# Kernel optimization log

Measured on AMD Instinct MI355X. Metric: run time of the kernel, lower is better.

Reference implementation:

```python
import jax, jax.numpy as jnp
import numpy as np

T, B, C, K, E = 1024, 32, 1024, 1024, 16  # seq, batch, d_model(=in=out), key_dim, n_experts
LOSS_SCALE = 0.01


def setup_inputs() -> dict:
    key0 = jax.random.key(0)
    k0, k1, k2, k3 = jax.random.split(key0, 4)
    x = jax.random.normal(k0, (T, B, C), dtype=jnp.float32)
    key = jax.random.normal(k1, (1, B, K), dtype=jnp.float32)
    bnd = float(np.sqrt(6.0 / (K + E)))  # xavier_uniform for assign Linear
    assign_w = jax.random.uniform(k2, (K, E), jnp.float32, -bnd, bnd)
    assign_b = jnp.zeros((E,), jnp.float32)
    a = float(np.sqrt(6.0) / (C + C))  # dynamic_init_method=1
    pw_w1 = jax.random.uniform(k3, (E, C * C), jnp.float32, -a, a)
    return {"x": x, "key": key, "assign_w": assign_w, "assign_b": assign_b, "pw_w1": pw_w1}


def reference(x, key, assign_w, assign_b, pw_w1):
    Tn, Bn, Cn = x.shape
    Tr = key.shape[0]  # key is provided -> Tr = 1 (one routing decision per batch element)
    En = assign_b.shape[0]
    # routing: softmax over experts (gumbel_tau=0 -> plain softmax branch)
    logits = key.reshape(Tr * Bn, -1) @ assign_w + assign_b  # (Tr*B, E)
    resp = jax.nn.softmax(logits, axis=-1)
    importance = resp.sum(axis=0)  # (E,)
    loss = LOSS_SCALE * jnp.std(importance, ddof=1) / jnp.mean(importance)  # torch.std is unbiased
    # mix expert weights: (Tr*B, E) @ (E, O*I) -> per-token/sentence weight matrix
    w = (resp @ pw_w1).reshape(Tr, Bn, Cn, Cn)  # (Tr, B, O, I)
    # batched matvec, broadcasting Tr=1 over T (sum over size-1 axis r == broadcast)
    y = jnp.einsum('rboi,tbi->tbo', w, x)
    return x + y, loss
```

## Files before the change

kernel.cpp:

```cpp
#include <hip/hip_runtime.h>
#include <stdint.h>


#define T_DIM 1024
#define B_DIM 32
#define C_DIM 1024
#define E_DIM 16
#define TBC   (1024*32*1024)

typedef __attribute__((ext_vector_type(8))) __bf16 bf16x8;
typedef __attribute__((ext_vector_type(4))) float  floatx4;

__device__ __forceinline__ unsigned short f2bf(float f) {
  unsigned u = __float_as_uint(f);
  unsigned r = u + 0x7fffu + ((u >> 16) & 1u);
  return (unsigned short)(r >> 16);
}

__device__ __forceinline__ void async16(const void* g, void* l) {
  __builtin_amdgcn_global_load_lds(
      (const __attribute__((address_space(1))) void*)(unsigned long long)(uintptr_t)g,
      (__attribute__((address_space(3))) void*)(unsigned int)(uintptr_t)l,
      16, 0, 0);
}

__global__ __launch_bounds__(256) void routing_kernel(
    const float* __restrict__ key, const float* __restrict__ aw,
    const float* __restrict__ ab, float* __restrict__ resp) {
  __shared__ float part[16][17];
  __shared__ float logit[16];
  const int b = blockIdx.x;
  const int tid = threadIdx.x;
  const int e = tid & 15, ks = tid >> 4;
  const float* kb = key + b * 1024 + ks * 64;
  float acc = 0.f;
  #pragma unroll 8
  for (int k = 0; k < 64; ++k)
    acc = fmaf(kb[k], aw[(ks * 64 + k) * 16 + e], acc);
  part[e][ks] = acc;
  __syncthreads();
  if (tid < 16) {
    float s = ab[tid];
    #pragma unroll
    for (int j = 0; j < 16; ++j) s += part[tid][j];
    logit[tid] = s;
  }
  __syncthreads();
  if (tid < 16) {
    float m = logit[0];
    #pragma unroll
    for (int j = 1; j < 16; ++j) m = fmaxf(m, logit[j]);
    float s = 0.f;
    #pragma unroll
    for (int j = 0; j < 16; ++j) s += expf(logit[j] - m);
    resp[b * 16 + tid] = expf(logit[tid] - m) / s;
  }
}

__global__ void loss_kernel(const float* __restrict__ resp, float* __restrict__ loss_out) {
  __shared__ float imp[16];
  const int tid = threadIdx.x;
  if (tid < 16) {
    float s = 0.f;
    for (int bb = 0; bb < 32; ++bb) s += resp[bb * 16 + tid];
    imp[tid] = s;
  }
  __syncthreads();
  if (tid == 0) {
    float mu = 0.f;
    for (int j = 0; j < 16; ++j) mu += imp[j];
    mu *= (1.f / 16.f);
    float var = 0.f;
    for (int j = 0; j < 16; ++j) { float d = imp[j] - mu; var += d * d; }
    var *= (1.f / 15.f);
    loss_out[0] = 0.01f * sqrtf(var) / mu;
  }
}

__global__ __launch_bounds__(256) void convert_kernel(
    const float4* __restrict__ x, ushort4* __restrict__ xb) {
  const int i = blockIdx.x * 256 + threadIdx.x;
  float4 v = x[i];
  ushort4 o;
  o.x = f2bf(v.x); o.y = f2bf(v.y); o.z = f2bf(v.z); o.w = f2bf(v.w);
  xb[i] = o;
}

__global__ __launch_bounds__(256) void mix_kernel(
    const float4* __restrict__ pw, const float* __restrict__ resp,
    ushort4* __restrict__ W) {
  __shared__ float rs[512];
  const int tid = threadIdx.x;
  rs[tid] = resp[tid];
  rs[tid + 256] = resp[tid + 256];
  __syncthreads();
  const int p = blockIdx.x * 256 + tid;
  float4 v[16];
  #pragma unroll
  for (int e = 0; e < 16; ++e) v[e] = pw[e * 262144 + p];
  #pragma unroll
  for (int b = 0; b < 32; ++b) {
    float ax = 0.f, ay = 0.f, az = 0.f, aww = 0.f;
    #pragma unroll
    for (int e = 0; e < 16; ++e) {
      const float r = rs[b * 16 + e];
      ax = fmaf(r, v[e].x, ax); ay = fmaf(r, v[e].y, ay);
      az = fmaf(r, v[e].z, az); aww = fmaf(r, v[e].w, aww);
    }
    ushort4 o;
    o.x = f2bf(ax); o.y = f2bf(ay); o.z = f2bf(az); o.w = f2bf(aww);
    W[(size_t)b * 262144 + p] = o;
  }
}

__global__ __launch_bounds__(256, 2) void gemm_kernel(
    const unsigned short* __restrict__ xb,
    const unsigned short* __restrict__ Wb,
    const float* __restrict__ xf,
    float* __restrict__ out) {
  __shared__ unsigned short lds[2 * 128 * 64];
  const int tid  = threadIdx.x;
  const int lane = tid & 63;
  const int wave = tid >> 6;
  const int wm = wave & 1, wn = wave >> 1;
  const int o0 = blockIdx.x * 128;
  const int t0 = blockIdx.y * 128;
  const int b  = blockIdx.z;

  unsigned short* ldsA = lds;
  unsigned short* ldsB = lds + 128 * 64;

  floatx4 acc[4][4];
  #pragma unroll
  for (int mi = 0; mi < 4; ++mi)
    #pragma unroll
    for (int ni = 0; ni < 4; ++ni)
      acc[mi][ni] = floatx4{0.f, 0.f, 0.f, 0.f};

  for (int kt = 0; kt < 1024; kt += 64) {
    if (kt) __syncthreads();
    #pragma unroll
    for (int j = 0; j < 4; ++j) {
      const int s  = j * 256 + tid;
      const int r  = s >> 3;
      const int cg = (s & 7) ^ (r & 7);
      const unsigned short* ga = xb + (size_t)(t0 + r) * 32768 + (size_t)b * 1024 + kt + cg * 8;
      async16(ga, ldsA + (size_t)(j * 256 + wave * 64) * 8);
      const unsigned short* gb = Wb + (size_t)b * 1048576 + (size_t)(o0 + r) * 1024 + kt + cg * 8;
      async16(gb, ldsB + (size_t)(j * 256 + wave * 64) * 8);
    }
    __syncthreads();
    #pragma unroll
    for (int kk = 0; kk < 2; ++kk) {
      bf16x8 af[4], bfr[4];
      #pragma unroll
      for (int mi = 0; mi < 4; ++mi) {
        const int r = wm * 64 + mi * 16 + (lane & 15);
        const int slot = (kk * 4 + (lane >> 4)) ^ (r & 7);
        af[mi] = *(const bf16x8*)(ldsA + r * 64 + slot * 8);
      }
      #pragma unroll
      for (int ni = 0; ni < 4; ++ni) {
        const int r = wn * 64 + ni * 16 + (lane & 15);
        const int slot = (kk * 4 + (lane >> 4)) ^ (r & 7);
        bfr[ni] = *(const bf16x8*)(ldsB + r * 64 + slot * 8);
      }
      #pragma unroll
      for (int mi = 0; mi < 4; ++mi)
        #pragma unroll
        for (int ni = 0; ni < 4; ++ni)
          acc[mi][ni] = __builtin_amdgcn_mfma_f32_16x16x32_bf16(af[mi], bfr[ni], acc[mi][ni], 0, 0, 0);
    }
  }

  #pragma unroll
  for (int mi = 0; mi < 4; ++mi) {
    const int tb = t0 + wm * 64 + mi * 16 + (lane >> 4) * 4;
    #pragma unroll
    for (int ni = 0; ni < 4; ++ni) {
      const int o = o0 + wn * 64 + ni * 16 + (lane & 15);
      #pragma unroll
      for (int v = 0; v < 4; ++v) {
        const size_t idx = (size_t)(tb + v) * 32768 + (size_t)b * 1024 + o;
        out[idx] = acc[mi][ni][v] + xf[idx];
      }
    }
  }
}

extern "C" void kernel_launch(void* const* d_in, const int* in_sizes, int n_in,
                              void* d_out, int out_size, void* d_ws, size_t ws_size,
                              hipStream_t stream) {
  const float* x   = (const float*)d_in[0];
  const float* key = (const float*)d_in[1];
  const float* aw  = (const float*)d_in[2];
  const float* ab  = (const float*)d_in[3];
  const float* pw  = (const float*)d_in[4];
  float* out = (float*)d_out;

  char* ws = (char*)d_ws;
  unsigned short* Wb = (unsigned short*)ws;
  unsigned short* xb = (unsigned short*)(ws + 67108864);
  float* resp        = (float*)(ws + 134217728);

  routing_kernel<<<32, 256, 0, stream>>>(key, aw, ab, resp);
  loss_kernel<<<1, 64, 0, stream>>>(resp, out + TBC);
  convert_kernel<<<32768, 256, 0, stream>>>((const float4*)x, (ushort4*)xb);
  mix_kernel<<<1024, 256, 0, stream>>>((const float4*)pw, resp, (ushort4*)Wb);
  gemm_kernel<<<dim3(8, 8, 32), 256, 0, stream>>>(xb, Wb, x, out);
}
```

Measured before the change: 419.5 us.

## Fuse small kernels, remap GEMM blocks per XCD, read residual from bf16 copy

Merges the routing and loss kernels into one 512-thread block, and merges the x conversion and expert-mixing kernels into one launch with branch-by-block-index. The GEMM now uses a 1D grid mapped so each XCD handles whole batch elements, aiming for better L2 reuse of that batch's weight matrix and activations. Global load pointers are hoisted out of the k-loop. The residual add reads the bf16 copy of x instead of the fp32 input, which halves residual read traffic but adds bf16 rounding error to the output's residual term.

```diff
diff --git a/kernel.cpp b/kernel.cpp
--- a/kernel.cpp
+++ b/kernel.cpp
@@ -2,10 +2,6 @@
 #include <stdint.h>
 
 
-#define T_DIM 1024
-#define B_DIM 32
-#define C_DIM 1024
-#define E_DIM 16
 #define TBC   (1024*32*1024)
 
 typedef __attribute__((ext_vector_type(8))) __bf16 bf16x8;
@@ -15,6 +11,9 @@
   unsigned u = __float_as_uint(f);
   unsigned r = u + 0x7fffu + ((u >> 16) & 1u);
   return (unsigned short)(r >> 16);
+}
+__device__ __forceinline__ float bf2f(unsigned short u) {
+  return __uint_as_float(((unsigned)u) << 16);
 }
 
 __device__ __forceinline__ void async16(const void* g, void* l) {
@@ -24,112 +23,126 @@
       16, 0, 0);
 }
 
-__global__ __launch_bounds__(256) void routing_kernel(
+__global__ __launch_bounds__(512) void routing_loss_kernel(
     const float* __restrict__ key, const float* __restrict__ aw,
-    const float* __restrict__ ab, float* __restrict__ resp) {
-  __shared__ float part[16][17];
-  __shared__ float logit[16];
-  const int b = blockIdx.x;
+    const float* __restrict__ ab, float* __restrict__ resp,
+    float* __restrict__ loss_out) {
+  __shared__ float logits[32][17];
+  __shared__ float respS[32][17];
+  __shared__ float imp[16];
   const int tid = threadIdx.x;
-  const int e = tid & 15, ks = tid >> 4;
-  const float* kb = key + b * 1024 + ks * 64;
+  const int e = tid & 15, b = tid >> 4;
+  const float4* k4 = (const float4*)(key + b * 1024);
   float acc = 0.f;
-  #pragma unroll 8
-  for (int k = 0; k < 64; ++k)
-    acc = fmaf(kb[k], aw[(ks * 64 + k) * 16 + e], acc);
-  part[e][ks] = acc;
+  #pragma unroll 4
+  for (int kk = 0; kk < 256; ++kk) {
+    const float4 kv = k4[kk];
+    const int k0 = kk * 4;
+    acc = fmaf(kv.x, aw[(k0 + 0) * 16 + e], acc);
+    acc = fmaf(kv.y, aw[(k0 + 1) * 16 + e], acc);
+    acc = fmaf(kv.z, aw[(k0 + 2) * 16 + e], acc);
+    acc = fmaf(kv.w, aw[(k0 + 3) * 16 + e], acc);
+  }
+  logits[b][e] = acc + ab[e];
+  __syncthreads();
+  float m = logits[b][0];
+  #pragma unroll
+  for (int j = 1; j < 16; ++j) m = fmaxf(m, logits[b][j]);
+  float s = 0.f;
+  #pragma unroll
+  for (int j = 0; j < 16; ++j) s += expf(logits[b][j] - m);
+  const float r = expf(logits[b][e] - m) / s;
+  respS[b][e] = r;
+  resp[b * 16 + e] = r;
   __syncthreads();
   if (tid < 16) {
-    float s = ab[tid];
-    #pragma unroll
-    for (int j = 0; j < 16; ++j) s += part[tid][j];
-    logit[tid] = s;
-  }
-  __syncthreads();
-  if (tid < 16) {
-    float m = logit[0];
-    #pragma unroll
-    for (int j = 1; j < 16; ++j) m = fmaxf(m, logit[j]);
-    float s = 0.f;
-    #pragma unroll
-    for (int j = 0; j < 16; ++j) s += expf(logit[j] - m);
-    resp[b * 16 + tid] = expf(logit[tid] - m) / s;
-  }
-}
-
-__global__ void loss_kernel(const float* __restrict__ resp, float* __restrict__ loss_out) {
-  __shared__ float imp[16];
-  const int tid = threadIdx.x;
-  if (tid < 16) {
-    float s = 0.f;
-    for (int bb = 0; bb < 32; ++bb) s += resp[bb * 16 + tid];
-    imp[tid] = s;
+    float si = 0.f;
+    #pragma unroll
+    for (int bb = 0; bb < 32; ++bb) si += respS[bb][tid];
+    imp[tid] = si;
   }
   __syncthreads();
   if (tid == 0) {
     float mu = 0.f;
+    #pragma unroll
     for (int j = 0; j < 16; ++j) mu += imp[j];
     mu *= (1.f / 16.f);
     float var = 0.f;
+    #pragma unroll
     for (int j = 0; j < 16; ++j) { float d = imp[j] - mu; var += d * d; }
     var *= (1.f / 15.f);
     loss_out[0] = 0.01f * sqrtf(var) / mu;
   }
 }
 
-__global__ __launch_bounds__(256) void convert_kernel(
-    const float4* __restrict__ x, ushort4* __restrict__ xb) {
-  const int i = blockIdx.x * 256 + threadIdx.x;
-  float4 v = x[i];
-  ushort4 o;
-  o.x = f2bf(v.x); o.y = f2bf(v.y); o.z = f2bf(v.z); o.w = f2bf(v.w);
-  xb[i] = o;
-}
-
-__global__ __launch_bounds__(256) void mix_kernel(
+__global__ __launch_bounds__(256) void prep_kernel(
+    const float4* __restrict__ x, ushort4* __restrict__ xb,
     const float4* __restrict__ pw, const float* __restrict__ resp,
     ushort4* __restrict__ W) {
-  __shared__ float rs[512];
   const int tid = threadIdx.x;
-  rs[tid] = resp[tid];
-  rs[tid + 256] = resp[tid + 256];
-  __syncthreads();
-  const int p = blockIdx.x * 256 + tid;
-  float4 v[16];
-  #pragma unroll
-  for (int e = 0; e < 16; ++e) v[e] = pw[e * 262144 + p];
-  #pragma unroll
-  for (int b = 0; b < 32; ++b) {
-    float ax = 0.f, ay = 0.f, az = 0.f, aww = 0.f;
-    #pragma unroll
-    for (int e = 0; e < 16; ++e) {
-      const float r = rs[b * 16 + e];
-      ax = fmaf(r, v[e].x, ax); ay = fmaf(r, v[e].y, ay);
-      az = fmaf(r, v[e].z, az); aww = fmaf(r, v[e].w, aww);
-    }
+  if (blockIdx.x < 32768) {
+    const int i = blockIdx.x * 256 + tid;
+    float4 v = x[i];
     ushort4 o;
-    o.x = f2bf(ax); o.y = f2bf(ay); o.z = f2bf(az); o.w = f2bf(aww);
-    W[(size_t)b * 262144 + p] = o;
+    o.x = f2bf(v.x); o.y = f2bf(v.y); o.z = f2bf(v.z); o.w = f2bf(v.w);
+    xb[i] = o;
+  } else {
+    __shared__ float rs[512];
+    rs[tid] = resp[tid];
+    rs[tid + 256] = resp[tid + 256];
+    __syncthreads();
+    const int p = (blockIdx.x - 32768) * 256 + tid;
+    float4 v[16];
+    #pragma unroll
+    for (int e = 0; e < 16; ++e) v[e] = pw[e * 262144 + p];
+    #pragma unroll
+    for (int b = 0; b < 32; ++b) {
+      float ax = 0.f, ay = 0.f, az = 0.f, aww = 0.f;
+      #pragma unroll
+      for (int e = 0; e < 16; ++e) {
+        const float r = rs[b * 16 + e];
+        ax = fmaf(r, v[e].x, ax); ay = fmaf(r, v[e].y, ay);
+        az = fmaf(r, v[e].z, az); aww = fmaf(r, v[e].w, aww);
+      }
+      ushort4 o;
+      o.x = f2bf(ax); o.y = f2bf(ay); o.z = f2bf(az); o.w = f2bf(aww);
+      W[(size_t)b * 262144 + p] = o;
+    }
   }
 }
 
 __global__ __launch_bounds__(256, 2) void gemm_kernel(
     const unsigned short* __restrict__ xb,
     const unsigned short* __restrict__ Wb,
-    const float* __restrict__ xf,
     float* __restrict__ out) {
   __shared__ unsigned short lds[2 * 128 * 64];
   const int tid  = threadIdx.x;
   const int lane = tid & 63;
   const int wave = tid >> 6;
   const int wm = wave & 1, wn = wave >> 1;
-  const int o0 = blockIdx.x * 128;
-  const int t0 = blockIdx.y * 128;
-  const int b  = blockIdx.z;
+
+  const int gid   = blockIdx.x;
+  const int xcd   = gid & 7;
+  const int local = gid >> 3;
+  const int b     = xcd * 4 + (local >> 6);
+  const int sub   = local & 63;
+  const int o0    = (sub & 7) * 128;
+  const int t0    = (sub >> 3) * 128;
 
   unsigned short* ldsA = lds;
   unsigned short* ldsB = lds + 128 * 64;
 
+  const unsigned short* gA[4];
+  const unsigned short* gB[4];
+  #pragma unroll
+  for (int j = 0; j < 4; ++j) {
+    const int s  = j * 256 + tid;
+    const int r  = s >> 3;
+    const int cg = (s & 7) ^ (r & 7);
+    gA[j] = xb + (size_t)(t0 + r) * 32768 + (size_t)b * 1024 + cg * 8;
+    gB[j] = Wb + (size_t)b * 1048576 + (size_t)(o0 + r) * 1024 + cg * 8;
+  }
+
   floatx4 acc[4][4];
   #pragma unroll
   for (int mi = 0; mi < 4; ++mi)
@@ -141,13 +154,9 @@
     if (kt) __syncthreads();
     #pragma unroll
     for (int j = 0; j < 4; ++j) {
-      const int s  = j * 256 + tid;
-      const int r  = s >> 3;
-      const int cg = (s & 7) ^ (r & 7);
-      const unsigned short* ga = xb + (size_t)(t0 + r) * 32768 + (size_t)b * 1024 + kt + cg * 8;
-      async16(ga, ldsA + (size_t)(j * 256 + wave * 64) * 8);
-      const unsigned short* gb = Wb + (size_t)b * 1048576 + (size_t)(o0 + r) * 1024 + kt + cg * 8;
-      async16(gb, ldsB + (size_t)(j * 256 + wave * 64) * 8);
+      async16(gA[j], ldsA + (size_t)(j * 256 + wave * 64) * 8);
+      async16(gB[j], ldsB + (size_t)(j * 256 + wave * 64) * 8);
+      gA[j] += 64; gB[j] += 64;
     }
     __syncthreads();
     #pragma unroll
@@ -182,7 +191,7 @@
       #pragma unroll
       for (int v = 0; v < 4; ++v) {
         const size_t idx = (size_t)(tb + v) * 32768 + (size_t)b * 1024 + o;
-        out[idx] = acc[mi][ni][v] + xf[idx];
+        out[idx] = acc[mi][ni][v] + bf2f(xb[idx]);
       }
     }
   }
@@ -203,9 +212,8 @@
   unsigned short* xb = (unsigned short*)(ws + 67108864);
   float* resp        = (float*)(ws + 134217728);
 
-  routing_kernel<<<32, 256, 0, stream>>>(key, aw, ab, resp);
-  loss_kernel<<<1, 64, 0, stream>>>(resp, out + TBC);
-  convert_kernel<<<32768, 256, 0, stream>>>((const float4*)x, (ushort4*)xb);
-  mix_kernel<<<1024, 256, 0, stream>>>((const float4*)pw, resp, (ushort4*)Wb);
-  gemm_kernel<<<dim3(8, 8, 32), 256, 0, stream>>>(xb, Wb, x, out);
-}
+  routing_loss_kernel<<<1, 512, 0, stream>>>(key, aw, ab, resp, out + TBC);
+  prep_kernel<<<33792, 256, 0, stream>>>((const float4*)x, (ushort4*)xb,
+                                         (const float4*)pw, resp, (ushort4*)Wb);
+  gemm_kernel<<<2048, 256, 0, stream>>>(xb, Wb, out);
+}
```

New measurement: 429.9 us. 1.02x slower.
